# Kernel optimization log

Hardware: AMD Instinct MI355X
Metric: run time of the kernel (lower is better)

The kernel has to match this reference:

```python
import jax, jax.numpy as jnp
import numpy as np

OBS, N, IN, H = 15, 50000, 2, 64
GX, GY = 4, 4
NS = 4.0


def setup_inputs() -> dict:
    key = jax.random.key(0)
    ks = jax.random.split(key, 15)
    tgt = jax.random.uniform(ks[0], (OBS, 1, IN), minval=-2.0, maxval=2.0, dtype=jnp.float32)
    oth = jax.random.uniform(ks[1], (OBS, N, IN), minval=-3.0, maxval=3.0, dtype=jnp.float32)
    mask = jax.random.randint(ks[2], (OBS, N), 0, 2, dtype=jnp.int32)
    s = 1.0 / np.sqrt(H)
    u = lambda k, shp: jax.random.uniform(k, shp, minval=-s, maxval=s, dtype=jnp.float32)
    return dict(
        observed_trajectory_target=tgt,
        observed_trajectory_others=oth,
        neighbor_mask=mask,
        W_ih=u(ks[3], (4 * H, IN)), b_ih=u(ks[4], (4 * H,)),
        W_hh=u(ks[5], (4 * H, H)), b_hh=u(ks[6], (4 * H,)),
        W1=u(ks[7], (H, H * GX * GY)), b1=u(ks[8], (H,)),
        W2=u(ks[9], (H, H)), b2=u(ks[10], (H,)),
        Wc=u(ks[11], (2, H)), bc=u(ks[12], (2,)),
    )


def reference(observed_trajectory_target, observed_trajectory_others, neighbor_mask,
              W_ih, b_ih, W_hh, b_hh, W1, b1, W2, b2, Wc, bc):
    cw = NS / GX   # cell width
    ch = NS / GY   # cell height
    hx, hy = GX // 2, GY // 2
    half = NS / 2.0

    def lstm_cell(x, h, c):
        # torch LSTMCell: gates ordered i, f, g, o
        gates = x @ W_ih.T + b_ih + h @ W_hh.T + b_hh
        i, f, g, o = jnp.split(gates, 4, axis=-1)
        c_new = jax.nn.sigmoid(f) * c + jax.nn.sigmoid(i) * jnp.tanh(g)
        h_new = jax.nn.sigmoid(o) * jnp.tanh(c_new)
        return h_new, c_new

    def step(carry, xs):
        h_t, c_t, h_o, c_o, _ = carry
        xt, xo, m = xs                      # xt: [2], xo: [N,2], m: [N]
        ref_pos = xt[:2]
        h_t, c_t = lstm_cell(xt[None, :], h_t, c_t)
        h_o, c_o = lstm_cell(xo, h_o, c_o)
        # social grid binning (dropout is identity in eval mode)
        rel = xo[:, :2] - ref_pos           # [N,2]
        within = (jnp.abs(rel[:, 0]) <= half) & (jnp.abs(rel[:, 1]) <= half)
        cx = jnp.trunc(rel[:, 0] / cw).astype(jnp.int32) + hx  # trunc == torch .long()
        cy = jnp.trunc(rel[:, 1] / ch).astype(jnp.int32) + hy
        valid = within & (cx >= 0) & (cx < GX) & (cy >= 0) & (cy < GY) & (m != 0)
        idx = jnp.where(valid, cy * GX + cx, 0)
        contrib = jnp.where(valid[:, None], h_o, 0.0)
        social = jax.ops.segment_sum(contrib, idx, num_segments=GX * GY)  # [16,H]
        sv = social.reshape(1, -1)          # [1, 16*H]
        ctx = jax.nn.relu(sv @ W1.T + b1) @ W2.T + b2
        combined = h_t + ctx
        return (h_t, c_t, h_o, c_o, combined), None

    Nn = observed_trajectory_others.shape[1]
    init = (jnp.zeros((1, H), jnp.float32), jnp.zeros((1, H), jnp.float32),
            jnp.zeros((Nn, H), jnp.float32), jnp.zeros((Nn, H), jnp.float32),
            jnp.zeros((1, H), jnp.float32))
    xs = (observed_trajectory_target[:, 0, :], observed_trajectory_others, neighbor_mask)
    (h_t, c_t, h_o, c_o, combined), _ = jax.lax.scan(step, init, xs)
    return combined @ Wc.T + bc  # [1, 2]
```

## Files before the change

### kernel.cpp

```cpp
#include <hip/hip_runtime.h>
#include <stdint.h>

#define OBS 15
#define NTOT 50000
#define HDIM 64
#define NPB 16
#define NBLK_N 3125
#define ZOFF (OBS * NPB * 8)

typedef __attribute__((ext_vector_type(8))) short short8;
typedef __attribute__((ext_vector_type(4))) float f32x4;
typedef __attribute__((ext_vector_type(4))) unsigned int u32x4;

static __device__ __forceinline__ unsigned short f2bf(float f) {
  unsigned u = __float_as_uint(f);
  u += 0x7fff + ((u >> 16) & 1);
  return (unsigned short)(u >> 16);
}
static __device__ __forceinline__ float bf2f(unsigned short b) {
  return __uint_as_float(((unsigned)b) << 16);
}

#if __has_builtin(__builtin_amdgcn_exp2f)
#define EXP2F(x) __builtin_amdgcn_exp2f(x)
#else
#define EXP2F(x) exp2f(x)
#endif
#if __has_builtin(__builtin_amdgcn_rcpf)
#define RCPF(x) __builtin_amdgcn_rcpf(x)
#else
#define RCPF(x) (1.0f / (x))
#endif

static __device__ __forceinline__ float sigm(float x) {
  return RCPF(1.0f + EXP2F(-1.4426950408889634f * x));
}
static __device__ __forceinline__ float tanh_(float x) {
  return 2.0f * RCPF(1.0f + EXP2F(-2.8853900817779268f * x)) - 1.0f;
}

static __device__ __forceinline__ int hidx(int r, int cb) {
  return r * 64 + ((cb ^ (r & 7)) << 3);
}

__global__ void k_zero(float* social) {
  social[threadIdx.x] = 0.0f;
}

#define MFMA_BF16 __builtin_amdgcn_mfma_f32_16x16x32_bf16

__global__ __launch_bounds__(256, 2)
void k_neigh(
    const float* __restrict__ tgt,
    const float* __restrict__ oth,
    const int* __restrict__ mask,
    const float* __restrict__ W_ih,
    const float* __restrict__ b_ih,
    const float* __restrict__ W_hh,
    const float* __restrict__ b_hh,
    float* __restrict__ social,
    float* __restrict__ ht_out)
{
  __shared__ __align__(16) unsigned short h2[2][NPB][HDIM];
  __shared__ __align__(16) unsigned short xbf[ZOFF + 8];
  __shared__ float xs14[NPB][2];
  __shared__ float tht[HDIM];
  __shared__ float tgb[256];

  const int tid = threadIdx.x;

  if (blockIdx.x == 0) {
    const float bias = b_ih[tid] + b_hh[tid];
    const float wi0 = W_ih[tid * 2], wi1 = W_ih[tid * 2 + 1];
    const float4* Wr = (const float4*)&W_hh[tid * 64];
    if (tid < HDIM) tht[tid] = 0.0f;
    float ct = 0.0f;
    __syncthreads();
    for (int t = 0; t < OBS; ++t) {
      const float x0 = tgt[t * 2], x1 = tgt[t * 2 + 1];
      float acc = bias + x0 * wi0 + x1 * wi1;
#pragma unroll 4
      for (int k4 = 0; k4 < 16; ++k4) {
        const float4 wv = Wr[k4];
        const float4 hv = *(const float4*)&tht[k4 * 4];
        acc += wv.x * hv.x + wv.y * hv.y + wv.z * hv.z + wv.w * hv.w;
      }
      tgb[tid] = acc;
      __syncthreads();
      if (tid < HDIM) {
        const float cn =
            sigm(tgb[64 + tid]) * ct + sigm(tgb[tid]) * tanh_(tgb[128 + tid]);
        ct = cn;
        tht[tid] = sigm(tgb[192 + tid]) * tanh_(cn);
      }
      __syncthreads();
    }
    if (tid < HDIM) ht_out[tid] = tht[tid];
    return;
  }

  const int l = tid & 63;
  const int w = tid >> 6;
  const int t15 = l & 15;
  const int g4 = l >> 4;
  const int n0 = (blockIdx.x - 1) * NPB;

  if (tid < OBS * NPB) {
    const int t = tid >> 4, n = tid & 15;
    const int gn = n0 + n;
    const float x0 = oth[(t * NTOT + gn) * 2 + 0];
    const float x1 = oth[(t * NTOT + gn) * 2 + 1];
    const unsigned short xh0 = f2bf(x0);
    const unsigned short xl0 = f2bf(x0 - bf2f(xh0));
    const unsigned short xh1 = f2bf(x1);
    const unsigned short xl1 = f2bf(x1 - bf2f(xh1));
    u32x4 d;
    d.x = (unsigned)xh0 | ((unsigned)xh0 << 16);
    d.y = (unsigned)xl0 | ((unsigned)xh1 << 16);
    d.z = (unsigned)xh1 | ((unsigned)xl1 << 16);
    d.w = 0x3F803F80u;
    *(u32x4*)&xbf[tid * 8] = d;
    if (t == OBS - 1) { xs14[n][0] = x0; xs14[n][1] = x1; }
  }
  if (tid == 255) {
    u32x4 zz = {0u, 0u, 0u, 0u};
    *(u32x4*)&xbf[ZOFF] = zz;
  }
  for (int i = tid; i < NPB * HDIM / 2; i += 256) ((unsigned int*)h2[0])[i] = 0u;

  short8 Bhi0, Bhi1, Bhi2, Bhi3, Bhi4, Bhi5, Bhi6, Bhi7;
  short8 Blo0, Blo1, Blo2, Blo3, Blo4, Blo5, Blo6, Blo7;
#define LOADB(q, kt, BH, BL)                                        \
  {                                                                 \
    const float* wp = &W_hh[(q * 64 + w * 16 + t15) * 64 + kt * 32 + g4 * 8]; \
    _Pragma("unroll") for (int j = 0; j < 8; ++j) {                 \
      float wv = wp[j];                                             \
      unsigned short hi = f2bf(wv);                                 \
      unsigned short lo = f2bf(wv - bf2f(hi));                      \
      BH[j] = (short)hi;                                            \
      BL[j] = (short)lo;                                            \
    }                                                               \
  }
  LOADB(0, 0, Bhi0, Blo0) LOADB(0, 1, Bhi1, Blo1)
  LOADB(1, 0, Bhi2, Blo2) LOADB(1, 1, Bhi3, Blo3)
  LOADB(2, 0, Bhi4, Blo4) LOADB(2, 1, Bhi5, Blo5)
  LOADB(3, 0, Bhi6, Blo6) LOADB(3, 1, Bhi7, Blo7)
#undef LOADB

  short8 BX0, BX1, BX2, BX3;
  {
    u32x4 z4 = {0u, 0u, 0u, 0u};
    BX0 = BX1 = BX2 = BX3 = __builtin_bit_cast(short8, z4);
    if (g4 == 0) {
#pragma unroll
      for (int q = 0; q < 4; ++q) {
        const int G = q * 64 + w * 16 + t15;
        const float w0 = W_ih[G * 2 + 0], w1 = W_ih[G * 2 + 1];
        const float bs = b_ih[G] + b_hh[G];
        const unsigned short w0h = f2bf(w0), w0l = f2bf(w0 - bf2f(w0h));
        const unsigned short w1h = f2bf(w1), w1l = f2bf(w1 - bf2f(w1h));
        const unsigned short bh = f2bf(bs), bl = f2bf(bs - bf2f(bh));
        u32x4 d;
        d.x = (unsigned)w0h | ((unsigned)w0l << 16);
        d.y = (unsigned)w0h | ((unsigned)w1h << 16);
        d.z = (unsigned)w1l | ((unsigned)w1h << 16);
        d.w = (unsigned)bh | ((unsigned)bl << 16);
        const short8 v = __builtin_bit_cast(short8, d);
        if (q == 0) BX0 = v;
        else if (q == 1) BX1 = v;
        else if (q == 2) BX2 = v;
        else BX3 = v;
      }
    }
  }

  int xo = (g4 == 0) ? (t15 * 8) : ZOFF;
  const int xst = (g4 == 0) ? (NPB * 8) : 0;

  f32x4 c = (f32x4){0.f, 0.f, 0.f, 0.f};
  const float refx = tgt[14 * 2 + 0];
  const float refy = tgt[14 * 2 + 1];

  __syncthreads();

  for (int t = 0; t < OBS; ++t) {
    const int cur = t & 1, nxt = cur ^ 1;
    const short8 Ax = *(const short8*)&xbf[xo];
    short8 A0 = *(const short8*)&h2[cur][0][hidx(t15, g4)];
    short8 A1 = *(const short8*)&h2[cur][0][hidx(t15, 4 + g4)];
    xo += xst;

    const f32x4 z = (f32x4){0.f, 0.f, 0.f, 0.f};
    f32x4 acc0 = MFMA_BF16(Ax, BX0, z, 0, 0, 0);
    f32x4 acc1 = MFMA_BF16(Ax, BX1, z, 0, 0, 0);
    f32x4 acc2 = MFMA_BF16(Ax, BX2, z, 0, 0, 0);
    f32x4 acc3 = MFMA_BF16(Ax, BX3, z, 0, 0, 0);
    acc0 = MFMA_BF16(A0, Bhi0, acc0, 0, 0, 0);
    acc1 = MFMA_BF16(A0, Bhi2, acc1, 0, 0, 0);
    acc2 = MFMA_BF16(A0, Bhi4, acc2, 0, 0, 0);
    acc3 = MFMA_BF16(A0, Bhi6, acc3, 0, 0, 0);
    acc0 = MFMA_BF16(A1, Bhi1, acc0, 0, 0, 0);
    acc1 = MFMA_BF16(A1, Bhi3, acc1, 0, 0, 0);
    acc2 = MFMA_BF16(A1, Bhi5, acc2, 0, 0, 0);
    acc3 = MFMA_BF16(A1, Bhi7, acc3, 0, 0, 0);
    acc0 = MFMA_BF16(A0, Blo0, acc0, 0, 0, 0);
    acc1 = MFMA_BF16(A0, Blo2, acc1, 0, 0, 0);
    acc2 = MFMA_BF16(A0, Blo4, acc2, 0, 0, 0);
    acc3 = MFMA_BF16(A0, Blo6, acc3, 0, 0, 0);
    acc0 = MFMA_BF16(A1, Blo1, acc0, 0, 0, 0);
    acc1 = MFMA_BF16(A1, Blo3, acc1, 0, 0, 0);
    acc2 = MFMA_BF16(A1, Blo5, acc2, 0, 0, 0);
    acc3 = MFMA_BF16(A1, Blo7, acc3, 0, 0, 0);

    if (t < OBS - 1) {
#pragma unroll
      for (int r = 0; r < 4; ++r) {
        float si = sigm(acc0[r]);
        float sf = sigm(acc1[r]);
        float tg = tanh_(acc2[r]);
        float so = sigm(acc3[r]);
        float cn = sf * c[r] + si * tg;
        c[r] = cn;
        float h = so * tanh_(cn);
        int n = g4 * 4 + r;
        int col = w * 16 + t15;
        h2[nxt][0][hidx(n, col >> 3) + (col & 7)] = f2bf(h);
      }
      __syncthreads();
    } else {
#pragma unroll
      for (int r = 0; r < 4; ++r) {
        float si = sigm(acc0[r]);
        float sf = sigm(acc1[r]);
        float tg = tanh_(acc2[r]);
        float so = sigm(acc3[r]);
        float cn = sf * c[r] + si * tg;
        float h = so * tanh_(cn);
        int nl = g4 * 4 + r;
        int gn = n0 + nl;
        float rx = xs14[nl][0] - refx;
        float ry = xs14[nl][1] - refy;
        bool within = (fabsf(rx) <= 2.0f) && (fabsf(ry) <= 2.0f);
        int cx = (int)truncf(rx) + 2;
        int cy = (int)truncf(ry) + 2;
        bool valid = within && (cx >= 0) && (cx < 4) && (cy >= 0) && (cy < 4);
        if (valid) {
          if (mask[(OBS - 1) * NTOT + gn] != 0)
            atomicAdd(&social[(cy * 4 + cx) * HDIM + w * 16 + t15], h);
        }
      }
    }
  }
}

__global__ __launch_bounds__(512) void k_final(
    const float* __restrict__ W1, const float* __restrict__ b1,
    const float* __restrict__ W2, const float* __restrict__ b2,
    const float* __restrict__ Wc, const float* __restrict__ bc,
    const float* __restrict__ social, const float* __restrict__ ht_g,
    float* __restrict__ out)
{
  __shared__ float sv[1024];
  __shared__ float hid[64];
  __shared__ float comb[64];
  __shared__ float ht[64];

  const int tid = threadIdx.x;
  for (int i = tid; i < 1024; i += 512) sv[i] = social[i];
  if (tid < 64) ht[tid] = ht_g[tid];
  __syncthreads();

  const int wv = tid >> 6, ln = tid & 63;
  for (int o = wv; o < 64; o += 8) {
    float p = 0.0f;
#pragma unroll
    for (int it = 0; it < 16; ++it) {
      const int j = it * 64 + ln;
      p += sv[j] * W1[o * 1024 + j];
    }
#pragma unroll
    for (int off = 32; off > 0; off >>= 1) p += __shfl_down(p, off);
    if (ln == 0) hid[o] = fmaxf(p + b1[o], 0.0f);
  }
  __syncthreads();
  for (int o = wv; o < 64; o += 8) {
    float p = hid[ln] * W2[o * 64 + ln];
#pragma unroll
    for (int off = 32; off > 0; off >>= 1) p += __shfl_down(p, off);
    if (ln == 0) comb[o] = ht[o] + p + b2[o];
  }
  __syncthreads();
  if (wv < 2) {
    float p = comb[ln] * Wc[wv * 64 + ln];
#pragma unroll
    for (int off = 32; off > 0; off >>= 1) p += __shfl_down(p, off);
    if (ln == 0) out[wv] = p + bc[wv];
  }
}

extern "C" void kernel_launch(void* const* d_in, const int* in_sizes, int n_in,
                              void* d_out, int out_size, void* d_ws, size_t ws_size,
                              hipStream_t stream) {
  const float* tgt = (const float*)d_in[0];
  const float* oth = (const float*)d_in[1];
  const int* mask = (const int*)d_in[2];
  const float* W_ih = (const float*)d_in[3];
  const float* b_ih = (const float*)d_in[4];
  const float* W_hh = (const float*)d_in[5];
  const float* b_hh = (const float*)d_in[6];
  const float* W1 = (const float*)d_in[7];
  const float* b1 = (const float*)d_in[8];
  const float* W2 = (const float*)d_in[9];
  const float* b2 = (const float*)d_in[10];
  const float* Wc = (const float*)d_in[11];
  const float* bc = (const float*)d_in[12];
  float* social = (float*)d_ws;
  float* ht = social + 1024;
  float* out = (float*)d_out;

  hipLaunchKernelGGL(k_zero, dim3(1), dim3(1024), 0, stream, social);
  hipLaunchKernelGGL(k_neigh, dim3(NBLK_N + 1), dim3(256), 0, stream,
                     tgt, oth, mask, W_ih, b_ih, W_hh, b_hh, social, ht);
  hipLaunchKernelGGL(k_final, dim3(1), dim3(512), 0, stream,
                     W1, b1, W2, b2, Wc, bc, social, ht, out);
}
```

Measured before the change: 126.1 us.

## Process 32 neighbors per block with two MFMA row tiles sharing weights

```diff
diff --git a/kernel.cpp b/kernel.cpp
--- a/kernel.cpp
+++ b/kernel.cpp
@@ -4,8 +4,8 @@
 #define OBS 15
 #define NTOT 50000
 #define HDIM 64
-#define NPB 16
-#define NBLK_N 3125
+#define NPB 32
+#define NBLK_N 1563
 #define ZOFF (OBS * NPB * 8)
 
 typedef __attribute__((ext_vector_type(8))) short short8;
@@ -105,11 +105,14 @@
   const int g4 = l >> 4;
   const int n0 = (blockIdx.x - 1) * NPB;
 
-  if (tid < OBS * NPB) {
-    const int t = tid >> 4, n = tid & 15;
+  for (int i = tid; i < OBS * NPB; i += 256) {
+    const int t = i >> 5, n = i & 31;
     const int gn = n0 + n;
-    const float x0 = oth[(t * NTOT + gn) * 2 + 0];
-    const float x1 = oth[(t * NTOT + gn) * 2 + 1];
+    float x0 = 0.0f, x1 = 0.0f;
+    if (gn < NTOT) {
+      const float2 xv = *(const float2*)&oth[(t * NTOT + gn) * 2];
+      x0 = xv.x; x1 = xv.y;
+    }
     const unsigned short xh0 = f2bf(x0);
     const unsigned short xl0 = f2bf(x0 - bf2f(xh0));
     const unsigned short xh1 = f2bf(x1);
@@ -119,7 +122,7 @@
     d.y = (unsigned)xl0 | ((unsigned)xh1 << 16);
     d.z = (unsigned)xh1 | ((unsigned)xl1 << 16);
     d.w = 0x3F803F80u;
-    *(u32x4*)&xbf[tid * 8] = d;
+    *(u32x4*)&xbf[i * 8] = d;
     if (t == OBS - 1) { xs14[n][0] = x0; xs14[n][1] = x1; }
   }
   if (tid == 255) {
@@ -176,8 +179,10 @@
 
   int xo = (g4 == 0) ? (t15 * 8) : ZOFF;
   const int xst = (g4 == 0) ? (NPB * 8) : 0;
-
-  f32x4 c = (f32x4){0.f, 0.f, 0.f, 0.f};
+  const int xg1 = (g4 == 0) ? (16 * 8) : 0;
+
+  f32x4 c0 = (f32x4){0.f, 0.f, 0.f, 0.f};
+  f32x4 c1 = (f32x4){0.f, 0.f, 0.f, 0.f};
   const float refx = tgt[14 * 2 + 0];
   const float refy = tgt[14 * 2 + 1];
 
@@ -185,70 +190,102 @@
 
   for (int t = 0; t < OBS; ++t) {
     const int cur = t & 1, nxt = cur ^ 1;
-    const short8 Ax = *(const short8*)&xbf[xo];
-    short8 A0 = *(const short8*)&h2[cur][0][hidx(t15, g4)];
-    short8 A1 = *(const short8*)&h2[cur][0][hidx(t15, 4 + g4)];
+    const unsigned short* hb = &h2[cur][0][0];
+    const short8 Ax0 = *(const short8*)&xbf[xo];
+    const short8 Ax1 = *(const short8*)&xbf[xo + xg1];
+    const short8 A00 = *(const short8*)&hb[hidx(t15, g4)];
+    const short8 A01 = *(const short8*)&hb[hidx(t15, 4 + g4)];
+    const short8 A10 = *(const short8*)&hb[hidx(16 + t15, g4)];
+    const short8 A11 = *(const short8*)&hb[hidx(16 + t15, 4 + g4)];
     xo += xst;
 
     const f32x4 z = (f32x4){0.f, 0.f, 0.f, 0.f};
-    f32x4 acc0 = MFMA_BF16(Ax, BX0, z, 0, 0, 0);
-    f32x4 acc1 = MFMA_BF16(Ax, BX1, z, 0, 0, 0);
-    f32x4 acc2 = MFMA_BF16(Ax, BX2, z, 0, 0, 0);
-    f32x4 acc3 = MFMA_BF16(Ax, BX3, z, 0, 0, 0);
-    acc0 = MFMA_BF16(A0, Bhi0, acc0, 0, 0, 0);
-    acc1 = MFMA_BF16(A0, Bhi2, acc1, 0, 0, 0);
-    acc2 = MFMA_BF16(A0, Bhi4, acc2, 0, 0, 0);
-    acc3 = MFMA_BF16(A0, Bhi6, acc3, 0, 0, 0);
-    acc0 = MFMA_BF16(A1, Bhi1, acc0, 0, 0, 0);
-    acc1 = MFMA_BF16(A1, Bhi3, acc1, 0, 0, 0);
-    acc2 = MFMA_BF16(A1, Bhi5, acc2, 0, 0, 0);
-    acc3 = MFMA_BF16(A1, Bhi7, acc3, 0, 0, 0);
-    acc0 = MFMA_BF16(A0, Blo0, acc0, 0, 0, 0);
-    acc1 = MFMA_BF16(A0, Blo2, acc1, 0, 0, 0);
-    acc2 = MFMA_BF16(A0, Blo4, acc2, 0, 0, 0);
-    acc3 = MFMA_BF16(A0, Blo6, acc3, 0, 0, 0);
-    acc0 = MFMA_BF16(A1, Blo1, acc0, 0, 0, 0);
-    acc1 = MFMA_BF16(A1, Blo3, acc1, 0, 0, 0);
-    acc2 = MFMA_BF16(A1, Blo5, acc2, 0, 0, 0);
-    acc3 = MFMA_BF16(A1, Blo7, acc3, 0, 0, 0);
+    f32x4 p0 = MFMA_BF16(Ax0, BX0, z, 0, 0, 0);
+    f32x4 p1 = MFMA_BF16(Ax0, BX1, z, 0, 0, 0);
+    f32x4 p2 = MFMA_BF16(Ax0, BX2, z, 0, 0, 0);
+    f32x4 p3 = MFMA_BF16(Ax0, BX3, z, 0, 0, 0);
+    f32x4 q0 = MFMA_BF16(Ax1, BX0, z, 0, 0, 0);
+    f32x4 q1 = MFMA_BF16(Ax1, BX1, z, 0, 0, 0);
+    f32x4 q2 = MFMA_BF16(Ax1, BX2, z, 0, 0, 0);
+    f32x4 q3 = MFMA_BF16(Ax1, BX3, z, 0, 0, 0);
+    p0 = MFMA_BF16(A00, Bhi0, p0, 0, 0, 0);
+    p1 = MFMA_BF16(A00, Bhi2, p1, 0, 0, 0);
+    p2 = MFMA_BF16(A00, Bhi4, p2, 0, 0, 0);
+    p3 = MFMA_BF16(A00, Bhi6, p3, 0, 0, 0);
+    q0 = MFMA_BF16(A10, Bhi0, q0, 0, 0, 0);
+    q1 = MFMA_BF16(A10, Bhi2, q1, 0, 0, 0);
+    q2 = MFMA_BF16(A10, Bhi4, q2, 0, 0, 0);
+    q3 = MFMA_BF16(A10, Bhi6, q3, 0, 0, 0);
+    p0 = MFMA_BF16(A01, Bhi1, p0, 0, 0, 0);
+    p1 = MFMA_BF16(A01, Bhi3, p1, 0, 0, 0);
+    p2 = MFMA_BF16(A01, Bhi5, p2, 0, 0, 0);
+    p3 = MFMA_BF16(A01, Bhi7, p3, 0, 0, 0);
+    q0 = MFMA_BF16(A11, Bhi1, q0, 0, 0, 0);
+    q1 = MFMA_BF16(A11, Bhi3, q1, 0, 0, 0);
+    q2 = MFMA_BF16(A11, Bhi5, q2, 0, 0, 0);
+    q3 = MFMA_BF16(A11, Bhi7, q3, 0, 0, 0);
+    p0 = MFMA_BF16(A00, Blo0, p0, 0, 0, 0);
+    p1 = MFMA_BF16(A00, Blo2, p1, 0, 0, 0);
+    p2 = MFMA_BF16(A00, Blo4, p2, 0, 0, 0);
+    p3 = MFMA_BF16(A00, Blo6, p3, 0, 0, 0);
+    q0 = MFMA_BF16(A10, Blo0, q0, 0, 0, 0);
+    q1 = MFMA_BF16(A10, Blo2, q1, 0, 0, 0);
+    q2 = MFMA_BF16(A10, Blo4, q2, 0, 0, 0);
+    q3 = MFMA_BF16(A10, Blo6, q3, 0, 0, 0);
+    p0 = MFMA_BF16(A01, Blo1, p0, 0, 0, 0);
+    p1 = MFMA_BF16(A01, Blo3, p1, 0, 0, 0);
+    p2 = MFMA_BF16(A01, Blo5, p2, 0, 0, 0);
+    p3 = MFMA_BF16(A01, Blo7, p3, 0, 0, 0);
+    q0 = MFMA_BF16(A11, Blo1, q0, 0, 0, 0);
+    q1 = MFMA_BF16(A11, Blo3, q1, 0, 0, 0);
+    q2 = MFMA_BF16(A11, Blo5, q2, 0, 0, 0);
+    q3 = MFMA_BF16(A11, Blo7, q3, 0, 0, 0);
 
     if (t < OBS - 1) {
+      unsigned short* hn = &h2[nxt][0][0];
+      const int col = w * 16 + t15;
 #pragma unroll
       for (int r = 0; r < 4; ++r) {
-        float si = sigm(acc0[r]);
-        float sf = sigm(acc1[r]);
-        float tg = tanh_(acc2[r]);
-        float so = sigm(acc3[r]);
-        float cn = sf * c[r] + si * tg;
-        c[r] = cn;
-        float h = so * tanh_(cn);
-        int n = g4 * 4 + r;
-        int col = w * 16 + t15;
-        h2[nxt][0][hidx(n, col >> 3) + (col & 7)] = f2bf(h);
+        {
+          const float si = sigm(p0[r]), sf = sigm(p1[r]);
+          const float tg = tanh_(p2[r]), so = sigm(p3[r]);
+          const float cn = sf * c0[r] + si * tg;
+          c0[r] = cn;
+          hn[hidx(g4 * 4 + r, col >> 3) + (col & 7)] = f2bf(so * tanh_(cn));
+        }
+        {
+          const float si = sigm(q0[r]), sf = sigm(q1[r]);
+          const float tg = tanh_(q2[r]), so = sigm(q3[r]);
+          const float cn = sf * c1[r] + si * tg;
+          c1[r] = cn;
+          hn[hidx(16 + g4 * 4 + r, col >> 3) + (col & 7)] =
+              f2bf(so * tanh_(cn));
+        }
       }
       __syncthreads();
     } else {
-#pragma unroll
-      for (int r = 0; r < 4; ++r) {
-        float si = sigm(acc0[r]);
-        float sf = sigm(acc1[r]);
-        float tg = tanh_(acc2[r]);
-        float so = sigm(acc3[r]);
-        float cn = sf * c[r] + si * tg;
-        float h = so * tanh_(cn);
-        int nl = g4 * 4 + r;
-        int gn = n0 + nl;
-        float rx = xs14[nl][0] - refx;
-        float ry = xs14[nl][1] - refy;
-        bool within = (fabsf(rx) <= 2.0f) && (fabsf(ry) <= 2.0f);
-        int cx = (int)truncf(rx) + 2;
-        int cy = (int)truncf(ry) + 2;
-        bool valid = within && (cx >= 0) && (cx < 4) && (cy >= 0) && (cy < 4);
-        if (valid) {
-          if (mask[(OBS - 1) * NTOT + gn] != 0)
-            atomicAdd(&social[(cy * 4 + cx) * HDIM + w * 16 + t15], h);
-        }
-      }
+#define POOL(P0, P1, P2, P3, C, G)                                         \
+  {                                                                        \
+    _Pragma("unroll") for (int r = 0; r < 4; ++r) {                        \
+      const float si = sigm(P0[r]), sf = sigm(P1[r]);                      \
+      const float tg = tanh_(P2[r]), so = sigm(P3[r]);                     \
+      const float cn = sf * C[r] + si * tg;                                \
+      const float h = so * tanh_(cn);                                      \
+      const int nl = G * 16 + g4 * 4 + r;                                  \
+      const int gn = n0 + nl;                                              \
+      const float rx = xs14[nl][0] - refx;                                 \
+      const float ry = xs14[nl][1] - refy;                                 \
+      bool ok = (fabsf(rx) <= 2.0f) && (fabsf(ry) <= 2.0f) && (gn < NTOT); \
+      const int cx = (int)truncf(rx) + 2;                   \
+      const int cy = (int)truncf(ry) + 2;                                  \
+      ok = ok && (cx >= 0) && (cx < 4) && (cy >= 0) && (cy < 4);           \
+      if (ok && mask[(OBS - 1) * NTOT + gn] != 0)                          \
+        atomicAdd(&social[(cy * 4 + cx) * HDIM + w * 16 + t15], h);        \
+    }                                                                      \
+  }
+      POOL(p0, p1, p2, p3, c0, 0)
+      POOL(q0, q1, q2, q3, c1, 1)
+#undef POOL
     }
   }
 }
```

Result: slower. 133.3 us (+5.7%).
